# Kernel optimization log

Hardware: AMD Instinct MI355X
Metric: run time of the kernel (lower is better)

## Reference

```python
import math
import jax, jax.numpy as jnp
import numpy as np

B, N, NC = 2, 2048, 256
C_S, C_COND, C_Z, C_H, H, PQK, PV = 384, 256, 128, 16, 12, 4, 8
BQ, BK = 32, 128
NBLK = N // BQ
INF, EPS = 1e5, 1e-8
CONCAT = C_Z // 4 + C_H + PV * 4  # per-head output feature dim


def _ln(x, w=None, b=None, eps=1e-5):
    mu = jnp.mean(x, -1, keepdims=True)
    var = jnp.mean((x - mu) ** 2, -1, keepdims=True)
    y = (x - mu) * jax.lax.rsqrt(var + eps)
    if w is not None:
        y = y * w
    if b is not None:
        y = y + b
    return y


def _quat_to_rot(q):
    w, x, y, z = q[..., 0], q[..., 1], q[..., 2], q[..., 3]
    r = jnp.stack([
        1 - 2 * (y * y + z * z), 2 * (x * y - w * z), 2 * (x * z + w * y),
        2 * (x * y + w * z), 1 - 2 * (x * x + z * z), 2 * (y * z - w * x),
        2 * (x * z - w * y), 2 * (y * z + w * x), 1 - 2 * (x * x + y * y),
    ], axis=-1)
    return r.reshape(q.shape[:-1] + (3, 3))


def setup_inputs() -> dict:
    key = jax.random.key(0)
    ks = jax.random.split(key, 24)
    p = lambda k, shp: 0.02 * jax.random.normal(k, shp, dtype=jnp.float32)
    quat = jax.random.normal(ks[5], (B, N, 4), dtype=jnp.float32)
    quat = quat / jnp.linalg.norm(quat, axis=-1, keepdims=True)
    hc = H * C_H
    return {
        "s": jax.random.normal(ks[0], (B, N, C_S), dtype=jnp.float32),
        "cond": jax.random.normal(ks[1], (B, NC, C_COND), dtype=jnp.float32),
        "z": jax.random.normal(ks[2], (B, NBLK, BQ, BK, C_Z), dtype=jnp.float32),
        "trans": jax.random.normal(ks[3], (B, N, 3), dtype=jnp.float32),
        "rots": _quat_to_rot(quat),
        "s_mask": jnp.ones((B, N), dtype=jnp.float32),
        "cond_to_s_idx": jax.random.randint(ks[4], (B, N), 0, NC),
        "ln_cond_w": jnp.ones((C_COND,), dtype=jnp.float32),
        "lin_cond_W": p(ks[6], (C_S, C_COND)),
        "lin_cond_b": jnp.zeros((C_S,), dtype=jnp.float32),
        "lin_cond_nb_W": p(ks[7], (C_S, C_COND)),
        "ln_z_w": jnp.ones((C_Z,), dtype=jnp.float32),
        "ln_z_b": jnp.zeros((C_Z,), dtype=jnp.float32),
        "Wq": p(ks[8], (hc, C_S)),
        "Wk": p(ks[9], (hc, C_S)),
        "Wv": p(ks[10], (hc, C_S)),
        "Wqp": p(ks[11], (H * PQK * 3, C_S)),
        "Wkvp": p(ks[12], (H * (PQK + PV) * 3, C_S)),
        "Wb": p(ks[13], (H, C_Z)),
        "Wdz": p(ks[14], (C_Z // 4, C_Z)),
        "head_weights": jnp.full((H,), 0.541324854612918, dtype=jnp.float32),
        "Wout": p(ks[15], (C_S, H * CONCAT)),
    }


def _forward(s, cond, z, trans, rots, s_mask, cond_to_s_idx,
             ln_cond_w, lin_cond_W, lin_cond_b, lin_cond_nb_W, ln_z_w, ln_z_b,
             Wq, Wk, Wv, Wqp, Wkvp, Wb, Wdz, head_weights, Wout):
    # ---- GatherAdaLN ----
    s_n = _ln(s)
    c_n = _ln(cond, ln_cond_w)
    idx3 = jnp.broadcast_to(cond_to_s_idx[..., None], (B, N, C_S))
    gate = jnp.take_along_axis(c_n @ lin_cond_W.T + lin_cond_b, idx3, axis=1) * s_mask[..., None]
    bias = jnp.take_along_axis(c_n @ lin_cond_nb_W.T, idx3, axis=1) * s_mask[..., None]
    s2 = s_n * jax.nn.sigmoid(gate) + bias
    # ---- pair LN ----
    zn = _ln(z, ln_z_w, ln_z_b)
    # ---- block gather (to_queries / to_keys) ----
    pad = (BK - BQ) // 2
    base = jnp.arange(NBLK)[:, None] * BQ + jnp.arange(BK)[None, :] - pad  # [NBLK, BK]
    validk = (base >= 0) & (base < N)
    kidx = jnp.clip(base, 0, N - 1)

    def to_q(x):
        return x.reshape((B, NBLK, BQ) + x.shape[2:])

    def to_k(x):
        g = x[:, kidx]  # [B, NBLK, BK, ...]
        vm = validk.reshape((1, NBLK, BK) + (1,) * (g.ndim - 3)).astype(g.dtype)
        return g * vm

    q_in, k_in = to_q(s2), to_k(s2)
    q_t, q_R = to_q(trans), to_q(rots)
    k_t = to_k(trans)
    k_R = jnp.where(validk[None, :, :, None, None], rots[:, kidx], jnp.eye(3, dtype=rots.dtype))
    # ---- scalar q/k/v ----
    q = (q_in @ Wq.T).reshape(B, NBLK, BQ, H, C_H)
    k = (k_in @ Wk.T).reshape(B, NBLK, BK, H, C_H)
    v = (k_in @ Wv.T).reshape(B, NBLK, BK, H, C_H)
    # ---- point q/k/v in global frames ----
    qp = (q_in @ Wqp.T).reshape(B, NBLK, BQ, H * PQK, 3)
    q_pts = (jnp.einsum('bnqij,bnqpj->bnqpi', q_R, qp) + q_t[..., None, :]).reshape(B, NBLK, BQ, H, PQK, 3)
    kvp = (k_in @ Wkvp.T).reshape(B, NBLK, BK, H * (PQK + PV), 3)
    kv_pts = (jnp.einsum('bnkij,bnkpj->bnkpi', k_R, kvp) + k_t[..., None, :]).reshape(B, NBLK, BK, H, PQK + PV, 3)
    k_pts, v_pts = kv_pts[..., :PQK, :], kv_pts[..., PQK:, :]
    # ---- logits ----
    b_bias = zn @ Wb.T  # [B,NBLK,BQ,BK,H]
    a = jnp.einsum('bnqhc,bnkhc->bnqkh', q, k) * math.sqrt(1.0 / (3 * C_H)) + b_bias * math.sqrt(1.0 / 3)
    # point bias (cdist form)
    pt = -2.0 * jnp.einsum('bnqhpd,bnkhpd->bnqkh', q_pts, k_pts)
    pt = pt + jnp.sum(q_pts ** 2, axis=(-1, -2))[..., None, :]
    pt = pt + jnp.sum(k_pts ** 2, axis=(-1, -2))[..., None, :, :]
    hw = jax.nn.softplus(head_weights) * math.sqrt(1.0 / (3 * (PQK * 9.0 / 2)))
    pt = pt * hw * (-0.5)
    qm = to_q(s_mask[..., None])  # [B,NBLK,BQ,1]
    km = to_k(s_mask[..., None])  # [B,NBLK,BK,1]
    amask = INF * (qm * jnp.swapaxes(km, -1, -2) - 1.0)  # [B,NBLK,BQ,BK]
    a = a + pt + amask[..., None]
    a = jax.nn.softmax(jnp.swapaxes(a, -1, -2), axis=-1)  # [B,NBLK,BQ,H,BK]
    # ---- outputs ----
    o = jnp.einsum('bnqhk,bnkhc->bnqhc', a, v).reshape(B, NBLK, BQ, H * C_H)
    o_pt = jnp.einsum('bnqhk,bnkhvc->bnqhvc', a, v_pts)
    o_pt = jnp.einsum('bnqij,bnqhvi->bnqhvj', q_R, o_pt - q_t[..., None, None, :])  # R^T (p - t)
    o_pt_norm = jnp.sqrt(jnp.sum(o_pt ** 2, -1) + EPS).reshape(B, NBLK, BQ, H * PV)
    o_pt_flat = o_pt.reshape(B, NBLK, BQ, H * PV * 3)
    pair_z = zn @ Wdz.T  # [B,NBLK,BQ,BK,C_Z//4]
    o_pair = jnp.einsum('bnqhk,bnqkc->bnqhc', a, pair_z).reshape(B, NBLK, BQ, H * (C_Z // 4))
    feats = jnp.concatenate([o, o_pt_flat, o_pt_norm, o_pair], axis=-1)
    return (feats @ Wout.T).reshape(B, N, C_S)


def reference(s, cond, z, trans, rots, s_mask, cond_to_s_idx,
              ln_cond_w, lin_cond_W, lin_cond_b, lin_cond_nb_W, ln_z_w, ln_z_b,
              Wq, Wk, Wv, Wqp, Wkvp, Wb, Wdz, head_weights, Wout):
    return _forward(s, cond, z, trans, rots, s_mask, cond_to_s_idx,
                    ln_cond_w, lin_cond_W, lin_cond_b, lin_cond_nb_W, ln_z_w, ln_z_b,
                    Wq, Wk, Wv, Wqp, Wkvp, Wb, Wdz, head_weights, Wout)
```

## Files before the change

### kernel.cpp

```cpp
#include <hip/hip_runtime.h>
#include <math.h>

constexpr int Bv = 2, Nv = 2048, NCv = 256;
constexpr int CSv = 384, CCONDv = 256;
constexpr int CHv = 16, Hv = 12, PQKv = 4, PVv = 8;
constexpr int BQv = 32, BKv = 128, NBLKv = 64;
constexpr int HC = Hv * CHv;
constexpr int QPD = Hv * PQKv * 3;
constexpr int FEAT = 960;
constexpr int PROJW = 1152;
constexpr float S1 = 0.14433756729740643f;
constexpr float S2 = 0.5773502691896258f;
constexpr float HWS = 0.13608276348795434f;

typedef __attribute__((ext_vector_type(8))) short bf16x8;
typedef __attribute__((ext_vector_type(4))) float f32x4;

__device__ __forceinline__ short f2bf(float f) {
    unsigned u = __float_as_uint(f);
    u += 0x7FFF + ((u >> 16) & 1);
    return (short)(u >> 16);
}
__device__ __forceinline__ float bf2f(short s) {
    return __uint_as_float(((unsigned)(unsigned short)s) << 16);
}
__device__ __forceinline__ unsigned pk2(short lo, short hi) {
    return ((unsigned)(unsigned short)lo) | (((unsigned)(unsigned short)hi) << 16);
}

__device__ __forceinline__ float blockReduceSum(float v, volatile float* red, int t, int nthr) {
    #pragma unroll
    for (int off = 32; off > 0; off >>= 1) v += __shfl_down(v, off, 64);
    int wid = t >> 6, lane = t & 63, nw = nthr >> 6;
    __syncthreads();
    if (lane == 0) red[wid] = v;
    __syncthreads();
    float r = 0.f;
    for (int w = 0; w < nw; ++w) r += red[w];
    return r;
}

__global__ __launch_bounds__(256) void k_wcvt(const float* __restrict__ Wq,
                                              const float* __restrict__ Wk,
                                              const float* __restrict__ Wv,
                                              const float* __restrict__ Wqp,
                                              const float* __restrict__ Wkvp,
                                              const float* __restrict__ Wg,
                                              const float* __restrict__ Wnb,
                                              short* __restrict__ wsW,
                                              short* __restrict__ wsW2) {
    int i4 = blockIdx.x * 256 + threadIdx.x;
    int off = i4 * 4;
    const float* src;
    short* dst;
    int rel;
    if (off < 442368) {
        dst = wsW; rel = off;
        if (rel < 73728) src = Wq;
        else if (rel < 147456) { src = Wk; rel -= 73728; }
        else if (rel < 221184) { src = Wv; rel -= 147456; }
        else if (rel < 276480) { src = Wqp; rel -= 221184; }
        else { src = Wkvp; rel -= 276480; }
        float4 v = *(const float4*)(src + rel);
        *(uint2*)(dst + off) = make_uint2(pk2(f2bf(v.x), f2bf(v.y)), pk2(f2bf(v.z), f2bf(v.w)));
    } else if (off < 442368 + 196608) {
        int o2 = off - 442368;
        rel = o2;
        if (rel < 98304) src = Wg; else { src = Wnb; rel -= 98304; }
        float4 v = *(const float4*)(src + rel);
        *(uint2*)(wsW2 + o2) = make_uint2(pk2(f2bf(v.x), f2bf(v.y)), pk2(f2bf(v.z), f2bf(v.w)));
    }
}

__global__ __launch_bounds__(256) void k_gemm_bt(const short* __restrict__ A,
                                                 const short* __restrict__ B,
                                                 float* __restrict__ C,
                                                 int K, int ldc) {
    __shared__ short As[128 * 40];
    __shared__ short Bs[128 * 40];
    int t = threadIdx.x;
    int m0 = blockIdx.x * 128, n0 = blockIdx.y * 128;
    int wv = t >> 6, lane = t & 63, lr = lane & 15, quad = lane >> 4;
    int mq = (wv & 1) * 64, nq = (wv >> 1) * 64;
    f32x4 acc[4][4];
    #pragma unroll
    for (int i = 0; i < 4; ++i)
        #pragma unroll
        for (int j = 0; j < 4; ++j) acc[i][j] = 0;

    int r0 = t >> 2, c8 = (t & 3) * 8;
    int r1 = (t + 256) >> 2, c81 = ((t + 256) & 3) * 8;

    for (int k0 = 0; k0 < K; k0 += 32) {
        uint4 a0 = *(const uint4*)(A + (size_t)(m0 + r0) * K + k0 + c8);
        uint4 a1 = *(const uint4*)(A + (size_t)(m0 + r1) * K + k0 + c81);
        uint4 b0 = *(const uint4*)(B + (size_t)(n0 + r0) * K + k0 + c8);
        uint4 b1 = *(const uint4*)(B + (size_t)(n0 + r1) * K + k0 + c81);
        *(uint4*)&As[r0 * 40 + c8] = a0;
        *(uint4*)&As[r1 * 40 + c81] = a1;
        *(uint4*)&Bs[r0 * 40 + c8] = b0;
        *(uint4*)&Bs[r1 * 40 + c81] = b1;
        __syncthreads();
        bf16x8 af[4], bf[4];
        #pragma unroll
        for (int i = 0; i < 4; ++i) {
            af[i] = *(const bf16x8*)&As[(mq + i * 16 + lr) * 40 + quad * 8];
            bf[i] = *(const bf16x8*)&Bs[(nq + i * 16 + lr) * 40 + quad * 8];
        }
        #pragma unroll
        for (int i = 0; i < 4; ++i)
            #pragma unroll
            for (int j = 0; j < 4; ++j)
                acc[i][j] = __builtin_amdgcn_mfma_f32_16x16x32_bf16(af[i], bf[j], acc[i][j], 0, 0, 0);
        __syncthreads();
    }
    #pragma unroll
    for (int i = 0; i < 4; ++i) {
        #pragma unroll
        for (int j = 0; j < 4; ++j) {
            int col = n0 + nq + j * 16 + lr;
            #pragma unroll
            for (int r = 0; r < 4; ++r) {
                int row = m0 + mq + i * 16 + quad * 4 + r;
                C[(size_t)row * ldc + col] = acc[i][j][r];
            }
        }
    }
}

__global__ __launch_bounds__(256) void k_condln(const float* __restrict__ cond,
                                                const float* __restrict__ lnw,
                                                short* __restrict__ cnbf) {
    __shared__ float red[4];
    int row = blockIdx.x;
    int t = threadIdx.x;
    float c = cond[row * CCONDv + t];
    float mu = blockReduceSum(c, red, t, 256) * (1.f / CCONDv);
    float d = c - mu;
    float var = blockReduceSum(d * d, red, t, 256) * (1.f / CCONDv);
    cnbf[row * CCONDv + t] = f2bf(d * rsqrtf(var + 1e-5f) * lnw[t]);
}

__global__ __launch_bounds__(128) void k_s2(const float* __restrict__ s,
                                            const float* __restrict__ gb,
                                            const float* __restrict__ bg,
                                            const int* __restrict__ cidx,
                                            const float* __restrict__ smask,
                                            short* __restrict__ s2bf) {
    __shared__ float red[4];
    int row = blockIdx.x;
    int t = threadIdx.x;
    const float* sr = s + (size_t)row * CSv;
    float x0 = sr[t], x1 = sr[t + 128], x2 = sr[t + 256];
    float mu = blockReduceSum(x0 + x1 + x2, red, t, 128) * (1.f / CSv);
    float d0 = x0 - mu, d1 = x1 - mu, d2 = x2 - mu;
    float var = blockReduceSum(d0 * d0 + d1 * d1 + d2 * d2, red, t, 128) * (1.f / CSv);
    float rs = rsqrtf(var + 1e-5f);
    int b = row / Nv;
    int ci = cidx[row];
    float m = smask[row];
    const float* gbr = gb + (size_t)(b * NCv + ci) * 768;
    float dd[3] = {d0, d1, d2};
    #pragma unroll
    for (int j = 0; j < 3; ++j) {
        int cc = t + j * 128;
        float sn = dd[j] * rs;
        float g = (gbr[cc] + bg[cc]) * m, bi = gbr[384 + cc] * m;
        s2bf[(size_t)row * CSv + cc] = f2bf(sn * (1.f / (1.f + expf(-g))) + bi);
    }
}

__global__ __launch_bounds__(192) void k_post(const float* __restrict__ proj,
                                              const float* __restrict__ rots,
                                              const float* __restrict__ trans,
                                              float* __restrict__ qpts,
                                              float* __restrict__ kpts,
                                              float* __restrict__ vpts,
                                              float* __restrict__ qsq,
                                              float* __restrict__ ksq) {
    __shared__ float R[9], tr[3];
    int row = blockIdx.x;
    int t = threadIdx.x;
    if (t < 9) R[t] = rots[(size_t)row * 9 + t];
    if (t < 3) tr[t] = trans[(size_t)row * 3 + t];
    __syncthreads();
    const float* pr = proj + (size_t)row * PROJW + 576;
    float x = pr[t * 3 + 0], y = pr[t * 3 + 1], z = pr[t * 3 + 2];
    float ox = R[0] * x + R[1] * y + R[2] * z + tr[0];
    float oy = R[3] * x + R[4] * y + R[5] * z + tr[1];
    float oz = R[6] * x + R[7] * y + R[8] * z + tr[2];
    float sq = ox * ox + oy * oy + oz * oz;
    if (t < 48) {
        qpts[(size_t)row * QPD + t * 3 + 0] = ox;
        qpts[(size_t)row * QPD + t * 3 + 1] = oy;
        qpts[(size_t)row * QPD + t * 3 + 2] = oz;
        float s4 = sq + __shfl_xor(sq, 1, 64);
        s4 += __shfl_xor(s4, 2, 64);
        if ((t & 3) == 0) qsq[(size_t)row * Hv + (t >> 2)] = s4;
    } else {
        int p = t - 48;
        int h = p / 12, pp = p % 12;
        if (pp < PQKv) {
            kpts[(size_t)row * QPD + (h * PQKv + pp) * 3 + 0] = ox;
            kpts[(size_t)row * QPD + (h * PQKv + pp) * 3 + 1] = oy;
            kpts[(size_t)row * QPD + (h * PQKv + pp) * 3 + 2] = oz;
            float s4 = sq + __shfl_xor(sq, 1, 64);
            s4 += __shfl_xor(s4, 2, 64);
            if (pp == 0) ksq[(size_t)row * Hv + h] = s4;
        } else {
            int vi = h * PVv + pp - PQKv;
            vpts[(size_t)row * (Hv * PVv * 3) + vi * 3 + 0] = ox;
            vpts[(size_t)row * (Hv * PVv * 3) + vi * 3 + 1] = oy;
            vpts[(size_t)row * (Hv * PVv * 3) + vi * 3 + 2] = oz;
        }
    }
}

__global__ __launch_bounds__(256) void k_prep(const float* __restrict__ Wb,
                                              const float* __restrict__ Wdz,
                                              const float* __restrict__ lnw,
                                              const float* __restrict__ lnb,
                                              short* __restrict__ wp,
                                              float* __restrict__ SB) {
    int t = threadIdx.x;
    if (t < 176) {
        int c = t >> 2, q = t & 3;
        const float* wrow = (c < 12) ? (Wb + (size_t)c * 128) : (Wdz + (size_t)(c - 12) * 128);
        float sacc = 0.f, bacc = 0.f;
        for (int i = q * 32; i < q * 32 + 32; ++i) {
            float wf = wrow[i] * lnw[i];
            short bs = f2bf(wf);
            wp[c * 128 + i] = bs;
            sacc += bf2f(bs);
            bacc += lnb[i] * wrow[i];
        }
        sacc += __shfl_xor(sacc, 1, 64); sacc += __shfl_xor(sacc, 2, 64);
        bacc += __shfl_xor(bacc, 1, 64); bacc += __shfl_xor(bacc, 2, 64);
        if (q == 0) { SB[c] = sacc; SB[48 + c] = bacc; }
    }
    for (int i = t; i < 512; i += 256) wp[44 * 128 + i] = 0;
    if (t >= 176 && t < 180) { SB[t - 132] = 0.f; SB[48 + t - 132] = 0.f; }
}

__global__ __launch_bounds__(256) void k_zproj2(const float* __restrict__ z,
                                                const short* __restrict__ wp,
                                                const float* __restrict__ SB,
                                                short* __restrict__ bbias2,
                                                short* __restrict__ pairzT) {
    __shared__ short zbuf[128 * 136];
    __shared__ short wbuf[48 * 136];
    __shared__ float muL[128], rsL[128], SL[48], BL[48];
    int t = threadIdx.x;
    int bid = blockIdx.x;
    int bblk = bid >> 5, qq = bid & 31;
    size_t row0 = (size_t)bid * 128;

    for (int idx = t; idx < 768; idx += 256) {
        int c = idx >> 4, k8 = idx & 15;
        uint4 v = *(const uint4*)(wp + c * 128 + k8 * 8);
        *(uint4*)&wbuf[c * 136 + k8 * 8] = v;
    }
    if (t < 96) {
        float v = SB[t];
        if (t < 48) SL[t] = v; else BL[t - 48] = v;
    }

    const float4* zsrc = (const float4*)(z + row0 * 128);
    #pragma unroll
    for (int it = 0; it < 16; ++it) {
        int f = it * 256 + t;
        int r = f >> 5, c4 = f & 31;
        float4 v = zsrc[f];
        short s0 = f2bf(v.x), s1 = f2bf(v.y), s2v = f2bf(v.z), s3 = f2bf(v.w);
        *(uint2*)&zbuf[r * 136 + c4 * 4] = make_uint2(pk2(s0, s1), pk2(s2v, s3));
        float sm = v.x + v.y + v.z + v.w;
        float sq = v.x * v.x + v.y * v.y + v.z * v.z + v.w * v.w;
        #pragma unroll
        for (int off = 1; off <= 16; off <<= 1) {
            sm += __shfl_xor(sm, off, 64);
            sq += __shfl_xor(sq, off, 64);
        }
        if ((t & 31) == 0) {
            float mu = sm * (1.f / 128.f);
            float var = sq * (1.f / 128.f) - mu * mu;
            muL[r] = mu;
            rsL[r] = rsqrtf(var + 1e-5f);
        }
    }
    __syncthreads();

    int wv = t >> 6, lane = t & 63;
    int lr = lane & 15, quad = lane >> 4;
    int mb = wv * 32;
    f32x4 acc[2][3];
    #pragma unroll
    for (int i = 0; i < 2; ++i)
        #pragma unroll
        for (int j = 0; j < 3; ++j) acc[i][j] = 0;
    #pragma unroll
    for (int kt = 0; kt < 4; ++kt) {
        int ko = kt * 32 + quad * 8;
        bf16x8 a0 = *(const bf16x8*)&zbuf[(mb + lr) * 136 + ko];
        bf16x8 a1 = *(const bf16x8*)&zbuf[(mb + 16 + lr) * 136 + ko];
        bf16x8 b0 = *(const bf16x8*)&wbuf[lr * 136 + ko];
        bf16x8 b1 = *(const bf16x8*)&wbuf[(16 + lr) * 136 + ko];
        bf16x8 b2 = *(const bf16x8*)&wbuf[(32 + lr) * 136 + ko];
        acc[0][0] = __builtin_amdgcn_mfma_f32_16x16x32_bf16(a0, b0, acc[0][0], 0, 0, 0);
        acc[0][1] = __builtin_amdgcn_mfma_f32_16x16x32_bf16(a0, b1, acc[0][1], 0, 0, 0);
        acc[0][2] = __builtin_amdgcn_mfma_f32_16x16x32_bf16(a0, b2, acc[0][2], 0, 0, 0);
        acc[1][0] = __builtin_amdgcn_mfma_f32_16x16x32_bf16(a1, b0, acc[1][0], 0, 0, 0);
        acc[1][1] = __builtin_amdgcn_mfma_f32_16x16x32_bf16(a1, b1, acc[1][1], 0, 0, 0);
        acc[1][2] = __builtin_amdgcn_mfma_f32_16x16x32_bf16(a1, b2, acc[1][2], 0, 0, 0);
    }

    short* bb_base = bbias2 + (size_t)(bblk * 12) * 4096 + qq * 128;
    short* pz_base = pairzT + (size_t)bid * 32 * 128;
    #pragma unroll
    for (int mt = 0; mt < 2; ++mt) {
        #pragma unroll
        for (int nt = 0; nt < 3; ++nt) {
            int col = nt * 16 + lr;
            int kbase = mb + mt * 16 + quad * 4;
            float ov[4];
            #pragma unroll
            for (int r4 = 0; r4 < 4; ++r4) {
                int rl = kbase + r4;
                ov[r4] = rsL[rl] * (acc[mt][nt][r4] - muL[rl] * SL[col]) + BL[col];
            }
            if (col < 12) {
                *(uint2*)&bb_base[(size_t)col * 4096 + kbase] =
                    make_uint2(pk2(f2bf(S2 * ov[0]), f2bf(S2 * ov[1])),
                               pk2(f2bf(S2 * ov[2]), f2bf(S2 * ov[3])));
            } else if (col < 44) {
                int c = col - 12;
                *(uint2*)&pz_base[c * 128 + kbase] =
                    make_uint2(pk2(f2bf(ov[0]), f2bf(ov[1])), pk2(f2bf(ov[2]), f2bf(ov[3])));
            }
        }
    }
}

__global__ __launch_bounds__(512, 6) void k_attn_main(const float* __restrict__ proj,
                                                      const float* __restrict__ qpts,
                                                      const float* __restrict__ kpts,
                                                      const float* __restrict__ vpts,
                                                      const float* __restrict__ qsq,
                                                      const float* __restrict__ ksq,
                                                      const short* __restrict__ bbias2,
                                                      const float* __restrict__ smask,
                                                      const float* __restrict__ head_w,
                                                      short* __restrict__ Aws,
                                                      float* __restrict__ optraw,
                                                      float* __restrict__ feats) {
    __shared__ short kfrag[128 * 40];
    __shared__ short qfrag[32 * 40];
    __shared__ short vtileT[48 * 136];
    __shared__ float sc[32 * 132];
    __shared__ short Abuf[32 * 136];
    __shared__ float rowb[32], qmL[32], colb[128], kmL[128];
    __shared__ int   nkgL[128];

    int t = threadIdx.x;
    int hp = blockIdx.x % 6;
    int bblk = blockIdx.x / 6;
    int b = bblk >> 6, blk = bblk & 63;
    int wv = t >> 6, lane = t & 63;
    int lr = lane & 15, quad = lane >> 4;

    if (t < 128) {
        int nkrel = blk * BQv + t - 48;
        bool valid = (nkrel >= 0) && (nkrel < Nv);
        int nkg = valid ? (b * Nv + nkrel) : -1;
        nkgL[t] = nkg;
        kmL[t] = valid ? smask[nkg] : 0.f;
    }
    {
        int c = 40 + (t >> 6), k2 = (t & 63) * 2;
        *(unsigned*)&vtileT[c * 136 + k2] = 0;
    }
    __syncthreads();

    for (int hh = 0; hh < 2; ++hh) {
        int h = hp * 2 + hh;
        float hw = log1pf(expf(head_w[h])) * HWS;

        {
            int k = t >> 2, c4 = (t & 3) << 2;
            int g = nkgL[k];
            float4 v = (g >= 0) ? *(const float4*)&proj[(size_t)g * PROJW + 192 + h * 16 + c4]
                                : make_float4(0, 0, 0, 0);
            *(uint2*)&kfrag[k * 40 + c4] =
                make_uint2(pk2(f2bf(v.x), f2bf(v.y)), pk2(f2bf(v.z), f2bf(v.w)));
            kfrag[k * 40 + 28 + (t & 3)] = 0;
        }
        if (t < 384) {
            int k = t / 3, c4 = (t % 3) * 4;
            int g = nkgL[k];
            float4 v = (g >= 0) ? *(const float4*)&kpts[(size_t)g * QPD + h * 12 + c4]
                                : make_float4(0, 0, 0, 0);
            *(uint2*)&kfrag[k * 40 + 16 + c4] =
                make_uint2(pk2(f2bf(v.x), f2bf(v.y)), pk2(f2bf(v.z), f2bf(v.w)));
        }
        if (t < 128) {
            int g = nkgL[t];
            colb[t] = (g >= 0) ? (-0.5f * hw * ksq[(size_t)g * Hv + h]) : 0.f;
            int q = t >> 2, c4 = (t & 3) << 2;
            int nqg = b * Nv + blk * BQv + q;
            float4 v = *(const float4*)&proj[(size_t)nqg * PROJW + h * 16 + c4];
            *(uint2*)&qfrag[q * 40 + c4] =
                make_uint2(pk2(f2bf(S1 * v.x), f2bf(S1 * v.y)),
                           pk2(f2bf(S1 * v.z), f2bf(S1 * v.w)));
            qfrag[q * 40 + 28 + (t & 3)] = 0;
        }
        if (t < 96) {
            int q = t / 3, c4 = (t % 3) * 4;
            int nqg = b * Nv + blk * BQv + q;
            float4 v = *(const float4*)&qpts[(size_t)nqg * QPD + h * 12 + c4];
            *(uint2*)&qfrag[q * 40 + 16 + c4] =
                make_uint2(pk2(f2bf(hw * v.x), f2bf(hw * v.y)),
                           pk2(f2bf(hw * v.z), f2bf(hw * v.w)));
        }
        if (t < 32) {
            int nqg = b * Nv + blk * BQv + t;
            rowb[t] = -0.5f * hw * qsq[(size_t)nqg * Hv + t >= 0 ? (size_t)nqg * Hv + h - ((size_t)nqg * Hv + h) + (size_t)nqg * Hv + h : 0];
            rowb[t] = -0.5f * hw * qsq[(size_t)nqg * Hv + h];
            qmL[t] = smask[nqg];
        }
        {
            int k = t >> 2, c0 = (t & 3) << 2;
            int g = nkgL[k];
            float4 v = (g >= 0) ? *(const float4*)&proj[(size_t)g * PROJW + 384 + h * 16 + c0]
                                : make_float4(0, 0, 0, 0);
            vtileT[(c0 + 0) * 136 + k] = f2bf(v.x);
            vtileT[(c0 + 1) * 136 + k] = f2bf(v.y);
            vtileT[(c0 + 2) * 136 + k] = f2bf(v.z);
            vtileT[(c0 + 3) * 136 + k] = f2bf(v.w);
        }
        for (int i = t; i < 768; i += 512) {
            int k = i / 6, p = i % 6;
            int g = nkgL[k];
            float4 v = (g >= 0) ? *(const float4*)&vpts[(size_t)g * (Hv * PVv * 3) + h * 24 + p * 4]
                                : make_float4(0, 0, 0, 0);
            int c0 = 16 + p * 4;
            vtileT[(c0 + 0) * 136 + k] = f2bf(v.x);
            vtileT[(c0 + 1) * 136 + k] = f2bf(v.y);
            vtileT[(c0 + 2) * 136 + k] = f2bf(v.z);
            vtileT[(c0 + 3) * 136 + k] = f2bf(v.w);
        }
        __syncthreads();

        f32x4 d[2];
        d[0] = 0; d[1] = 0;
        {
            bf16x8 bfr = *(const bf16x8*)&kfrag[(wv * 16 + lr) * 40 + quad * 8];
            bf16x8 a0 = *(const bf16x8*)&qfrag[lr * 40 + quad * 8];
            bf16x8 a1 = *(const bf16x8*)&qfrag[(16 + lr) * 40 + quad * 8];
            d[0] = __builtin_amdgcn_mfma_f32_16x16x32_bf16(a0, bfr, d[0], 0, 0, 0);
            d[1] = __builtin_amdgcn_mfma_f32_16x16x32_bf16(a1, bfr, d[1], 0, 0, 0);
        }
        {
            const short* bb = bbias2 + (size_t)(bblk * 12 + h) * 4096;
            #pragma unroll
            for (int mt = 0; mt < 2; ++mt) {
                #pragma unroll
                for (int r = 0; r < 4; ++r) {
                    int q = mt * 16 + quad * 4 + r;
                    int k = wv * 16 + lr;
                    float logit = d[mt][r] + rowb[q] + colb[k]
                                + 1e5f * (qmL[q] * kmL[k] - 1.f)
                                + bf2f(bb[q * 128 + k]);
                    sc[q * 132 + k] = logit;
                }
            }
        }
        __syncthreads();

        {
            int q = t >> 4, i0 = (t & 15) * 8;
            float v[8];
            float m = -3.0e38f;
            #pragma unroll
            for (int j = 0; j < 8; ++j) { v[j] = sc[q * 132 + i0 + j]; m = fmaxf(m, v[j]); }
            #pragma unroll
            for (int off = 1; off <= 8; off <<= 1) m = fmaxf(m, __shfl_xor(m, off, 64));
            float ssum = 0.f;
            #pragma unroll
            for (int j = 0; j < 8; ++j) { v[j] = __expf(v[j] - m); ssum += v[j]; }
            #pragma unroll
            for (int off = 1; off <= 8; off <<= 1) ssum += __shfl_xor(ssum, off, 64);
            float inv = 1.f / ssum;
            short a8[8];
            #pragma unroll
            for (int j = 0; j < 8; ++j) a8[j] = f2bf(v[j] * inv);
            uint4 packed = make_uint4(pk2(a8[0], a8[1]), pk2(a8[2], a8[3]),
                                      pk2(a8[4], a8[5]), pk2(a8[6], a8[7]));
            *(uint4*)&Abuf[q * 136 + i0] = packed;
            *(uint4*)&Aws[((size_t)(bblk * 32 + q) * 12 + h) * 128 + i0] = packed;
        }
        __syncthreads();

        if (wv < 6) {
            int mt = wv & 1, nt = wv >> 1;
            f32x4 acc = 0;
            #pragma unroll
            for (int kt = 0; kt < 4; ++kt) {
                bf16x8 a = *(const bf16x8*)&Abuf[(mt * 16 + lr) * 136 + quad * 8 + kt * 32];
                bf16x8 bv = *(const bf16x8*)&vtileT[(nt * 16 + lr) * 136 + quad * 8 + kt * 32];
                acc = __builtin_amdgcn_mfma_f32_16x16x32_bf16(a, bv, acc, 0, 0, 0);
            }
            int c = nt * 16 + lr;
            #pragma unroll
            for (int r = 0; r < 4; ++r) {
                int q = mt * 16 + quad * 4 + r;
                size_t nqg = (size_t)b * Nv + blk * BQv + q;
                if (c < 16) feats[nqg * FEAT + h * 16 + c] = acc[r];
                else if (c < 40) optraw[nqg * 288 + h * 24 + (c - 16)] = acc[r];
            }
        }
        __syncthreads();
    }
}

__global__ __launch_bounds__(64) void k_pair(const short* __restrict__ Aws,
                                             const short* __restrict__ pairzT,
                                             const float* __restrict__ optraw,
                                             const float* __restrict__ rots,
                                             const float* __restrict__ trans,
                                             float* __restrict__ feats) {
    __shared__ float Rt[12];
    int t = threadIdx.x;
    int bid = blockIdx.x;
    int lr = t & 15, quad = t >> 4;

    if (t < 9) Rt[t] = rots[(size_t)bid * 9 + t];
    if (t < 3) Rt[9 + t] = trans[(size_t)bid * 3 + t];
    __syncthreads();

    const short* Ab = Aws + (size_t)bid * 1536;
    const short* Pb = pairzT + (size_t)bid * 4096;
    f32x4 acc0 = 0, acc1 = 0;
    #pragma unroll
    for (int kt = 0; kt < 4; ++kt) {
        int ko = kt * 32 + quad * 8;
        bf16x8 a = 0;
        if (lr < 12) a = *(const bf16x8*)&Ab[lr * 128 + ko];
        bf16x8 b0 = *(const bf16x8*)&Pb[lr * 128 + ko];
        bf16x8 b1 = *(const bf16x8*)&Pb[(16 + lr) * 128 + ko];
        acc0 = __builtin_amdgcn_mfma_f32_16x16x32_bf16(a, b0, acc0, 0, 0, 0);
        acc1 = __builtin_amdgcn_mfma_f32_16x16x32_bf16(a, b1, acc1, 0, 0, 0);
    }
    float* frow = feats + (size_t)bid * FEAT;
    #pragma unroll
    for (int r = 0; r < 4; ++r) {
        int hh = quad * 4 + r;
        if (hh < 12) {
            frow[576 + hh * 32 + lr] = acc0[r];
            frow[576 + hh * 32 + 16 + lr] = acc1[r];
        }
    }

    for (int p = t; p < 96; p += 64) {
        float x = optraw[(size_t)bid * 288 + p * 3 + 0] - Rt[9];
        float y = optraw[(size_t)bid * 288 + p * 3 + 1] - Rt[10];
        float z = optraw[(size_t)bid * 288 + p * 3 + 2] - Rt[11];
        float lx = Rt[0] * x + Rt[3] * y + Rt[6] * z;
        float ly = Rt[1] * x + Rt[4] * y + Rt[7] * z;
        float lz = Rt[2] * x + Rt[5] * y + Rt[8] * z;
        frow[192 + p * 3 + 0] = lx;
        frow[192 + p * 3 + 1] = ly;
        frow[192 + p * 3 + 2] = lz;
        frow[480 + p] = sqrtf(lx * lx + ly * ly + lz * lz + 1e-8f);
    }
}

__global__ __launch_bounds__(256) void k_out(const float* __restrict__ A,
                                             const float* __restrict__ Wo,
                                             float* __restrict__ C) {
    __shared__ float As[32][65];
    __shared__ float Bs[32][65];
    int t = threadIdx.x;
    int m0 = blockIdx.x * 64;
    int c0 = blockIdx.y * 64;
    int tx = t & 15, ty = t >> 4;
    int lr = t >> 2, lk = (t & 3) * 8;
    float acc[4][4] = {};
    for (int k0 = 0; k0 < FEAT; k0 += 32) {
        const float4* ap = (const float4*)(A + (size_t)(m0 + lr) * FEAT + k0 + lk);
        const float4* bp = (const float4*)(Wo + (size_t)(c0 + lr) * FEAT + k0 + lk);
        float4 a0 = ap[0], a1 = ap[1];
        float4 b0 = bp[0], b1 = bp[1];
        As[lk + 0][lr] = a0.x; As[lk + 1][lr] = a0.y; As[lk + 2][lr] = a0.z; As[lk + 3][lr] = a0.w;
        As[lk + 4][lr] = a1.x; As[lk + 5][lr] = a1.y; As[lk + 6][lr] = a1.z; As[lk + 7][lr] = a1.w;
        Bs[lk + 0][lr] = b0.x; Bs[lk + 1][lr] = b0.y; Bs[lk + 2][lr] = b0.z; Bs[lk + 3][lr] = b0.w;
        Bs[lk + 4][lr] = b1.x; Bs[lk + 5][lr] = b1.y; Bs[lk + 6][lr] = b1.z; Bs[lk + 7][lr] = b1.w;
        __syncthreads();
        #pragma unroll
        for (int kk = 0; kk < 32; ++kk) {
            float a4[4], b4[4];
            #pragma unroll
            for (int i = 0; i < 4; ++i) a4[i] = As[kk][ty * 4 + i];
            #pragma unroll
            for (int j = 0; j < 4; ++j) b4[j] = Bs[kk][tx * 4 + j];
            #pragma unroll
            for (int i = 0; i < 4; ++i)
                #pragma unroll
                for (int j = 0; j < 4; ++j) acc[i][j] += a4[i] * b4[j];
        }
        __syncthreads();
    }
    #pragma unroll
    for (int i = 0; i < 4; ++i)
        #pragma unroll
        for (int j = 0; j < 4; ++j)
            C[(size_t)(m0 + ty * 4 + i) * CSv + c0 + tx * 4 + j] = acc[i][j];
}

extern "C" void kernel_launch(void* const* d_in, const int* in_sizes, int n_in,
                              void* d_out, int out_size, void* d_ws, size_t ws_size,
                              hipStream_t stream) {
    const float* s          = (const float*)d_in[0];
    const float* cond       = (const float*)d_in[1];
    const float* z          = (const float*)d_in[2];
    const float* trans      = (const float*)d_in[3];
    const float* rots       = (const float*)d_in[4];
    const float* smask      = (const float*)d_in[5];
    const int*   cidx       = (const int*)d_in[6];
    const float* ln_cond_w  = (const float*)d_in[7];
    const float* lin_cond_W = (const float*)d_in[8];
    const float* lin_cond_b = (const float*)d_in[9];
    const float* lin_cond_nb_W = (const float*)d_in[10];
    const float* ln_z_w     = (const float*)d_in[11];
    const float* ln_z_b     = (const float*)d_in[12];
    const float* Wq         = (const float*)d_in[13];
    const float* Wk         = (const float*)d_in[14];
    const float* Wv         = (const float*)d_in[15];
    const float* Wqp        = (const float*)d_in[16];
    const float* Wkvp       = (const float*)d_in[17];
    const float* Wb         = (const float*)d_in[18];
    const float* Wdz        = (const float*)d_in[19];
    const float* head_w     = (const float*)d_in[20];
    const float* Wout       = (const float*)d_in[21];
    float* out = (float*)d_out;

    float* p = (float*)d_ws;
    short* wp = (short*)p; p += 3072;
    float* SBp = p; p += 96;
    short* wsW  = (short*)p; p += 221184;
    short* wsW2 = (short*)p; p += 98304;
    short* cnbf = (short*)p; p += 65536;
    float* gb   = p; p += (size_t)512 * 768;
    short* s2bf = (short*)p; p += (size_t)Bv * Nv * CSv / 2;
    float* proj = p; p += (size_t)Bv * Nv * PROJW;
    float* qpts = p; p += (size_t)Bv * Nv * QPD;
    float* kpts = p; p += (size_t)Bv * Nv * QPD;
    float* vpts = p; p += (size_t)Bv * Nv * (Hv * PVv * 3);
    float* qsq  = p; p += (size_t)Bv * Nv * Hv;
    float* ksq  = p; p += (size_t)Bv * Nv * Hv;
    short* bbias2 = (short*)p; p += (size_t)128 * 12 * 4096 / 2;
    short* pairzT = (short*)p; p += (size_t)128 * 32 * 32 * 64;
    short* Aws    = (short*)p; p += (size_t)4096 * 12 * 64;
    float* optraw = p; p += (size_t)4096 * 288;
    float* feats  = p; p += (size_t)Bv * Nv * FEAT;

    k_wcvt<<<624, 256, 0, stream>>>(Wq, Wk, Wv, Wqp, Wkvp, lin_cond_W, lin_cond_nb_W,
                                    wsW, wsW2);
    k_prep<<<1, 256, 0, stream>>>(Wb, Wdz, ln_z_w, ln_z_b, wp, SBp);
    k_condln<<<Bv * NCv, 256, 0, stream>>>(cond, ln_cond_w, cnbf);
    k_gemm_bt<<<dim3(4, 6), 256, 0, stream>>>(cnbf, wsW2, gb, CCONDv, 768);
    k_s2<<<Bv * Nv, 128, 0, stream>>>(s, gb, lin_cond_b, cidx, smask, s2bf);
    k_gemm_bt<<<dim3(32, 9), 256, 0, stream>>>(s2bf, wsW, proj, CSv, PROJW);
    k_post<<<Bv * Nv, 192, 0, stream>>>(proj, rots, trans, qpts, kpts, vpts, qsq, ksq);
    k_zproj2<<<Bv * NBLKv * BQv, 256, 0, stream>>>(z, wp, SBp, bbias2, pairzT);
    k_attn_main<<<Bv * NBLKv * 6, 512, 0, stream>>>(proj, qpts, kpts, vpts, qsq, ksq,
                                                    bbias2, smask, head_w, Aws, optraw, feats);
    k_pair<<<Bv * NBLKv * BQv, 64, 0, stream>>>(Aws, pairzT, optraw, rots, trans, feats);
    k_out<<<dim3(64, 6), 256, 0, stream>>>(feats, Wout, out);
}
```

Measured before the change: 616.8 us.

## Fuse setup kernels, merge cond GEMM into z-projection, precompute bf16 K/Q/V tiles

Folds the weight conversion, z-LN weight prep and cond LayerNorm into one launch, and runs the small cond GEMM as extra blocks of the z-projection kernel. Adds a k_kvcache pass that converts K/Q/V and point features to bf16 once per (batch, head) into padded, pre-transposed buffers. The attention kernel then loads those tiles with plain 16-byte copies, avoiding repeated fp32 gathers and conversions across overlapping key windows. It also pads the k_out shared tiles and vectorises their reads. The cost is one extra kernel, extra workspace traffic for the cached buffers, and fewer launches overall.

```diff
diff --git a/kernel.cpp b/kernel.cpp
--- a/kernel.cpp
+++ b/kernel.cpp
@@ -9,6 +9,7 @@
 constexpr int QPD = Hv * PQKv * 3;
 constexpr int FEAT = 960;
 constexpr int PROJW = 1152;
+constexpr int NPAD = 2144;
 constexpr float S1 = 0.14433756729740643f;
 constexpr float S2 = 0.5773502691896258f;
 constexpr float HWS = 0.13608276348795434f;
@@ -27,6 +28,8 @@
 __device__ __forceinline__ unsigned pk2(short lo, short hi) {
     return ((unsigned)(unsigned short)lo) | (((unsigned)(unsigned short)hi) << 16);
 }
+
+union BF8 { short s[8]; bf16x8 v; uint4 u; };
 
 __device__ __forceinline__ float blockReduceSum(float v, volatile float* red, int t, int nthr) {
     #pragma unroll
@@ -40,7 +43,7 @@
     return r;
 }
 
-__global__ __launch_bounds__(256) void k_wcvt(const float* __restrict__ Wq,
+__global__ __launch_bounds__(256) void k_head(const float* __restrict__ Wq,
                                               const float* __restrict__ Wk,
                                               const float* __restrict__ Wv,
                                               const float* __restrict__ Wqp,
@@ -48,27 +51,64 @@
                                               const float* __restrict__ Wg,
                                               const float* __restrict__ Wnb,
                                               short* __restrict__ wsW,
-                                              short* __restrict__ wsW2) {
-    int i4 = blockIdx.x * 256 + threadIdx.x;
-    int off = i4 * 4;
-    const float* src;
-    short* dst;
-    int rel;
-    if (off < 442368) {
-        dst = wsW; rel = off;
-        if (rel < 73728) src = Wq;
-        else if (rel < 147456) { src = Wk; rel -= 73728; }
-        else if (rel < 221184) { src = Wv; rel -= 147456; }
-        else if (rel < 276480) { src = Wqp; rel -= 221184; }
-        else { src = Wkvp; rel -= 276480; }
-        float4 v = *(const float4*)(src + rel);
-        *(uint2*)(dst + off) = make_uint2(pk2(f2bf(v.x), f2bf(v.y)), pk2(f2bf(v.z), f2bf(v.w)));
-    } else if (off < 442368 + 196608) {
-        int o2 = off - 442368;
-        rel = o2;
-        if (rel < 98304) src = Wg; else { src = Wnb; rel -= 98304; }
-        float4 v = *(const float4*)(src + rel);
-        *(uint2*)(wsW2 + o2) = make_uint2(pk2(f2bf(v.x), f2bf(v.y)), pk2(f2bf(v.z), f2bf(v.w)));
+                                              short* __restrict__ wsW2,
+                                              const float* __restrict__ Wb,
+                                              const float* __restrict__ Wdz,
+                                              const float* __restrict__ lnzw,
+                                              const float* __restrict__ lnzb,
+                                              short* __restrict__ wp,
+                                              float* __restrict__ SB,
+                                              const float* __restrict__ cond,
+                                              const float* __restrict__ lncw,
+                                              short* __restrict__ cnbf) {
+    __shared__ float red[4];
+    int bid = blockIdx.x;
+    int t = threadIdx.x;
+    if (bid < 624) {
+        int off = (bid * 256 + t) * 4;
+        const float* src;
+        int rel;
+        if (off < 442368) {
+            rel = off;
+            if (rel < 73728) src = Wq;
+            else if (rel < 147456) { src = Wk; rel -= 73728; }
+            else if (rel < 221184) { src = Wv; rel -= 147456; }
+            else if (rel < 276480) { src = Wqp; rel -= 221184; }
+            else { src = Wkvp; rel -= 276480; }
+            float4 v = *(const float4*)(src + rel);
+            *(uint2*)(wsW + off) = make_uint2(pk2(f2bf(v.x), f2bf(v.y)), pk2(f2bf(v.z), f2bf(v.w)));
+        } else {
+            int o2 = off - 442368;
+            rel = o2;
+            if (rel < 98304) src = Wg; else { src = Wnb; rel -= 98304; }
+            float4 v = *(const float4*)(src + rel);
+            *(uint2*)(wsW2 + o2) = make_uint2(pk2(f2bf(v.x), f2bf(v.y)), pk2(f2bf(v.z), f2bf(v.w)));
+        }
+    } else if (bid == 624) {
+        if (t < 176) {
+            int c = t >> 2, q = t & 3;
+            const float* wrow = (c < 12) ? (Wb + (size_t)c * 128) : (Wdz + (size_t)(c - 12) * 128);
+            float sacc = 0.f, bacc = 0.f;
+            for (int i = q * 32; i < q * 32 + 32; ++i) {
+                float wf = wrow[i] * lnzw[i];
+                short bs = f2bf(wf);
+                wp[c * 128 + i] = bs;
+                sacc += bf2f(bs);
+                bacc += lnzb[i] * wrow[i];
+            }
+            sacc += __shfl_xor(sacc, 1, 64); sacc += __shfl_xor(sacc, 2, 64);
+            bacc += __shfl_xor(bacc, 1, 64); bacc += __shfl_xor(bacc, 2, 64);
+            if (q == 0) { SB[c] = sacc; SB[48 + c] = bacc; }
+        }
+        for (int i = t; i < 512; i += 256) wp[44 * 128 + i] = 0;
+        if (t >= 176 && t < 180) { SB[t - 132] = 0.f; SB[48 + t - 132] = 0.f; }
+    } else {
+        int row = bid - 625;
+        float c = cond[row * CCONDv + t];
+        float mu = blockReduceSum(c, red, t, 256) * (1.f / CCONDv);
+        float d = c - mu;
+        float var = blockReduceSum(d * d, red, t, 256) * (1.f / CCONDv);
+        cnbf[row * CCONDv + t] = f2bf(d * rsqrtf(var + 1e-5f) * lncw[t]);
     }
 }
 
@@ -126,19 +166,6 @@
             }
         }
     }
-}
-
-__global__ __launch_bounds__(256) void k_condln(const float* __restrict__ cond,
-                                                const float* __restrict__ lnw,
-                                                short* __restrict__ cnbf) {
-    __shared__ float red[4];
-    int row = blockIdx.x;
-    int t = threadIdx.x;
-    float c = cond[row * CCONDv + t];
-    float mu = blockReduceSum(c, red, t, 256) * (1.f / CCONDv);
-    float d = c - mu;
-    float var = blockReduceSum(d * d, red, t, 256) * (1.f / CCONDv);
-    cnbf[row * CCONDv + t] = f2bf(d * rsqrtf(var + 1e-5f) * lnw[t]);
 }
 
 __global__ __launch_bounds__(128) void k_s2(const float* __restrict__ s,
@@ -216,42 +243,75 @@
     }
 }
 
-__global__ __launch_bounds__(256) void k_prep(const float* __restrict__ Wb,
-                                              const float* __restrict__ Wdz,
-                                              const float* __restrict__ lnw,
-                                              const float* __restrict__ lnb,
-                                              short* __restrict__ wp,
-                                              float* __restrict__ SB) {
-    int t = threadIdx.x;
-    if (t < 176) {
-        int c = t >> 2, q = t & 3;
-        const float* wrow = (c < 12) ? (Wb + (size_t)c * 128) : (Wdz + (size_t)(c - 12) * 128);
-        float sacc = 0.f, bacc = 0.f;
-        for (int i = q * 32; i < q * 32 + 32; ++i) {
-            float wf = wrow[i] * lnw[i];
-            short bs = f2bf(wf);
-            wp[c * 128 + i] = bs;
-            sacc += bf2f(bs);
-            bacc += lnb[i] * wrow[i];
-        }
-        sacc += __shfl_xor(sacc, 1, 64); sacc += __shfl_xor(sacc, 2, 64);
-        bacc += __shfl_xor(bacc, 1, 64); bacc += __shfl_xor(bacc, 2, 64);
-        if (q == 0) { SB[c] = sacc; SB[48 + c] = bacc; }
-    }
-    for (int i = t; i < 512; i += 256) wp[44 * 128 + i] = 0;
-    if (t >= 176 && t < 180) { SB[t - 132] = 0.f; SB[48 + t - 132] = 0.f; }
-}
-
-__global__ __launch_bounds__(256) void k_zproj2(const float* __restrict__ z,
-                                                const short* __restrict__ wp,
-                                                const float* __restrict__ SB,
-                                                short* __restrict__ bbias2,
-                                                short* __restrict__ pairzT) {
-    __shared__ short zbuf[128 * 136];
-    __shared__ short wbuf[48 * 136];
-    __shared__ float muL[128], rsL[128], SL[48], BL[48];
+__global__ __launch_bounds__(256) void k_zg(const float* __restrict__ z,
+                                            const short* __restrict__ wp,
+                                            const float* __restrict__ SB,
+                                            short* __restrict__ bbias2,
+                                            short* __restrict__ pairzT,
+                                            const short* __restrict__ cnbf,
+                                            const short* __restrict__ wsW2,
+                                            float* __restrict__ gb) {
+    extern __shared__ char smem[];
     int t = threadIdx.x;
     int bid = blockIdx.x;
+    if (bid >= 4096) {
+        short* As = (short*)smem;
+        short* Bs = As + 128 * 40;
+        int g = bid - 4096;
+        int m0 = (g & 3) * 128, n0 = (g >> 2) * 128;
+        const int K = CCONDv, ldc = 768;
+        int wv = t >> 6, lane = t & 63, lr = lane & 15, quad = lane >> 4;
+        int mq = (wv & 1) * 64, nq = (wv >> 1) * 64;
+        f32x4 acc[4][4];
+        #pragma unroll
+        for (int i = 0; i < 4; ++i)
+            #pragma unroll
+            for (int j = 0; j < 4; ++j) acc[i][j] = 0;
+        int r0 = t >> 2, c8 = (t & 3) * 8;
+        int r1 = (t + 256) >> 2, c81 = ((t + 256) & 3) * 8;
+        for (int k0 = 0; k0 < K; k0 += 32) {
+            uint4 a0 = *(const uint4*)(cnbf + (size_t)(m0 + r0) * K + k0 + c8);
+            uint4 a1 = *(const uint4*)(cnbf + (size_t)(m0 + r1) * K + k0 + c81);
+            uint4 b0 = *(const uint4*)(wsW2 + (size_t)(n0 + r0) * K + k0 + c8);
+            uint4 b1 = *(const uint4*)(wsW2 + (size_t)(n0 + r1) * K + k0 + c81);
+            *(uint4*)&As[r0 * 40 + c8] = a0;
+            *(uint4*)&As[r1 * 40 + c81] = a1;
+            *(uint4*)&Bs[r0 * 40 + c8] = b0;
+            *(uint4*)&Bs[r1 * 40 + c81] = b1;
+            __syncthreads();
+            bf16x8 af[4], bf[4];
+            #pragma unroll
+            for (int i = 0; i < 4; ++i) {
+                af[i] = *(const bf16x8*)&As[(mq + i * 16 + lr) * 40 + quad * 8];
+                bf[i] = *(const bf16x8*)&Bs[(nq + i * 16 + lr) * 40 + quad * 8];
+            }
+            #pragma unroll
+            for (int i = 0; i < 4; ++i)
+                #pragma unroll
+                for (int j = 0; j < 4; ++j)
+                    acc[i][j] = __builtin_amdgcn_mfma_f32_16x16x32_bf16(af[i], bf[j], acc[i][j], 0, 0, 0);
+            __syncthreads();
+        }
+        #pragma unroll
+        for (int i = 0; i < 4; ++i)
+            #pragma unroll
+            for (int j = 0; j < 4; ++j) {
+                int col = n0 + nq + j * 16 + lr;
+                #pragma unroll
+                for (int r = 0; r < 4; ++r) {
+                    int row = m0 + mq + i * 16 + quad * 4 + r;
+                    gb[(size_t)row * ldc + col] = acc[i][j][r];
+                }
+            }
+        return;
+    }
+    short* zbuf = (short*)smem;
+    short* wbuf = zbuf + 128 * 136;
+    float* muL  = (float*)(wbuf + 48 * 136);
+    float* rsL  = muL + 128;
+    float* SL   = rsL + 128;
+    float* BL   = SL + 48;
+
     int bblk = bid >> 5, qq = bid & 31;
     size_t row0 = (size_t)bid * 128;
 
@@ -340,15 +400,111 @@
     }
 }
 
-__global__ __launch_bounds__(512, 6) void k_attn_main(const float* __restrict__ proj,
-                                                      const float* __restrict__ qpts,
-                                                      const float* __restrict__ kpts,
-                                                      const float* __restrict__ vpts,
-                                                      const float* __restrict__ qsq,
-                                                      const float* __restrict__ ksq,
+__global__ __launch_bounds__(256) void k_kvcache(const float* __restrict__ proj,
+                                                 const float* __restrict__ qpts,
+                                                 const float* __restrict__ kpts,
+                                                 const float* __restrict__ vpts,
+                                                 const float* __restrict__ qsq,
+                                                 const float* __restrict__ ksq,
+                                                 const float* __restrict__ smask,
+                                                 const float* __restrict__ head_w,
+                                                 short* __restrict__ kc,
+                                                 short* __restrict__ qc,
+                                                 short* __restrict__ vTc,
+                                                 float* __restrict__ cb,
+                                                 float* __restrict__ rb,
+                                                 float* __restrict__ kmp) {
+    __shared__ short vt[40 * 136];
+    int t = threadIdx.x;
+    int tile = blockIdx.x % 17;
+    int bh = blockIdx.x / 17;
+    int b = bh / 12, h = bh % 12;
+    float hw = log1pf(expf(head_w[h])) * HWS;
+    int pn0 = tile * 128;
+    int npn = (pn0 + 128 <= NPAD) ? 128 : (NPAD - pn0);
+
+    for (int i = t; i < npn * 4; i += 256) {
+        int r = i >> 2, q = i & 3;
+        int pn = pn0 + r;
+        int n = pn - 48; n = n < 0 ? 0 : (n > Nv - 1 ? Nv - 1 : n);
+        size_t g = (size_t)b * Nv + n;
+        BF8 o;
+        if (q < 2) {
+            const float* src = proj + g * PROJW + 192 + h * 16 + q * 8;
+            #pragma unroll
+            for (int j = 0; j < 8; ++j) o.s[j] = f2bf(src[j]);
+        } else if (q == 2) {
+            const float* src = kpts + g * QPD + h * 12;
+            #pragma unroll
+            for (int j = 0; j < 8; ++j) o.s[j] = f2bf(src[j]);
+        } else {
+            const float* src = kpts + g * QPD + h * 12 + 8;
+            #pragma unroll
+            for (int j = 0; j < 4; ++j) o.s[j] = f2bf(src[j]);
+            o.s[4] = o.s[5] = o.s[6] = o.s[7] = 0;
+        }
+        *(uint4*)&kc[(((size_t)bh) * NPAD + pn) * 32 + q * 8] = o.u;
+    }
+    for (int i = t; i < npn; i += 256) {
+        int pn = pn0 + i;
+        int n = pn - 48; n = n < 0 ? 0 : (n > Nv - 1 ? Nv - 1 : n);
+        size_t g = (size_t)b * Nv + n;
+        cb[(size_t)bh * NPAD + pn] = -0.5f * hw * ksq[g * Hv + h];
+        if (h == 0) kmp[(size_t)b * NPAD + pn] = (pn >= 48 && pn < 48 + Nv) ? smask[g] : 0.f;
+    }
+    for (int i = t; i < 512; i += 256) {
+        int r = i >> 2, q = i & 3;
+        int n = pn0 - 48 + r;
+        if (n >= 0 && n < Nv) {
+            size_t g = (size_t)b * Nv + n;
+            BF8 o;
+            if (q < 2) {
+                const float* src = proj + g * PROJW + h * 16 + q * 8;
+                #pragma unroll
+                for (int j = 0; j < 8; ++j) o.s[j] = f2bf(S1 * src[j]);
+            } else if (q == 2) {
+                const float* src = qpts + g * QPD + h * 12;
+                #pragma unroll
+                for (int j = 0; j < 8; ++j) o.s[j] = f2bf(hw * src[j]);
+            } else {
+                const float* src = qpts + g * QPD + h * 12 + 8;
+                #pragma unroll
+                for (int j = 0; j < 4; ++j) o.s[j] = f2bf(hw * src[j]);
+                o.s[4] = o.s[5] = o.s[6] = o.s[7] = 0;
+            }
+            *(uint4*)&qc[(((size_t)bh) * Nv + n) * 32 + q * 8] = o.u;
+            if (q == 0) rb[(size_t)bh * Nv + n] = -0.5f * hw * qsq[g * Hv + h];
+        }
+    }
+    for (int i = t; i < npn * 10; i += 256) {
+        int r = i / 10, q = i % 10;
+        int pn = pn0 + r;
+        int n = pn - 48; n = n < 0 ? 0 : (n > Nv - 1 ? Nv - 1 : n);
+        size_t g = (size_t)b * Nv + n;
+        float4 v = (q < 4) ? *(const float4*)&proj[g * PROJW + 384 + h * 16 + q * 4]
+                           : *(const float4*)&vpts[g * (Hv * PVv * 3) + h * 24 + (q - 4) * 4];
+        int c0 = q * 4;
+        vt[(c0 + 0) * 136 + r] = f2bf(v.x);
+        vt[(c0 + 1) * 136 + r] = f2bf(v.y);
+        vt[(c0 + 2) * 136 + r] = f2bf(v.z);
+        vt[(c0 + 3) * 136 + r] = f2bf(v.w);
+    }
+    __syncthreads();
+    for (int i = t; i < 640; i += 256) {
+        int c = i >> 4, s = i & 15;
+        if (s * 8 < npn)
+            *(uint4*)&vTc[((size_t)bh * 40 + c) * NPAD + pn0 + s * 8] = *(const uint4*)&vt[c * 136 + s * 8];
+    }
+}
+
+__global__ __launch_bounds__(512, 6) void k_attn_main(const short* __restrict__ kc,
+                                                      const short* __restrict__ qc,
+                                                      const short* __restrict__ vTc,
+                                                      const float* __restrict__ cb,
+                                                      const float* __restrict__ rb,
+                                                      const float* __restrict__ kmp,
+                                                      const float* __restrict__ smask,
                                                       const short* __restrict__ bbias2,
-                                                      const float* __restrict__ smask,
-                                                      const float* __restrict__ head_w,
                                                       short* __restrict__ Aws,
                                                       float* __restrict__ optraw,
                                                       float* __restrict__ feats) {
@@ -358,7 +514,6 @@
     __shared__ float sc[32 * 132];
     __shared__ short Abuf[32 * 136];
     __shared__ float rowb[32], qmL[32], colb[128], kmL[128];
-    __shared__ int   nkgL[128];
 
     int t = threadIdx.x;
     int hp = blockIdx.x % 6;
@@ -366,14 +521,10 @@
     int b = bblk >> 6, blk = bblk & 63;
     int wv = t >> 6, lane = t & 63;
     int lr = lane & 15, quad = lane >> 4;
-
-    if (t < 128) {
-        int nkrel = blk * BQv + t - 48;
-        bool valid = (nkrel >= 0) && (nkrel < Nv);
-        int nkg = valid ? (b * Nv + nkrel) : -1;
-        nkgL[t] = nkg;
-        kmL[t] = valid ? smask[nkg] : 0.f;
-    }
+    int n0 = blk * BQv;
+
+    if (t < 128) kmL[t] = kmp[(size_t)b * NPAD + n0 + t];
+    if (t < 32)  qmL[t] = smask[(size_t)b * Nv + n0 + t];
     {
         int c = 40 + (t >> 6), k2 = (t & 63) * 2;
         *(unsigned*)&vtileT[c * 136 + k2] = 0;
@@ -382,70 +533,21 @@
 
     for (int hh = 0; hh < 2; ++hh) {
         int h = hp * 2 + hh;
-        float hw = log1pf(expf(head_w[h])) * HWS;
+        size_t bh = (size_t)b * 12 + h;
 
         {
-            int k = t >> 2, c4 = (t & 3) << 2;
-            int g = nkgL[k];
-            float4 v = (g >= 0) ? *(const float4*)&proj[(size_t)g * PROJW + 192 + h * 16 + c4]
-                                : make_float4(0, 0, 0, 0);
-            *(uint2*)&kfrag[k * 40 + c4] =
-                make_uint2(pk2(f2bf(v.x), f2bf(v.y)), pk2(f2bf(v.z), f2bf(v.w)));
-            kfrag[k * 40 + 28 + (t & 3)] = 0;
-        }
-        if (t < 384) {
-            int k = t / 3, c4 = (t % 3) * 4;
-            int g = nkgL[k];
-            float4 v = (g >= 0) ? *(const float4*)&kpts[(size_t)g * QPD + h * 12 + c4]
-                                : make_float4(0, 0, 0, 0);
-            *(uint2*)&kfrag[k * 40 + 16 + c4] =
-                make_uint2(pk2(f2bf(v.x), f2bf(v.y)), pk2(f2bf(v.z), f2bf(v.w)));
+            int r = t >> 2, s8 = (t & 3) * 8;
+            *(uint4*)&kfrag[r * 40 + s8] = *(const uint4*)&kc[(bh * NPAD + n0 + r) * 32 + s8];
         }
         if (t < 128) {
-            int g = nkgL[t];
-            colb[t] = (g >= 0) ? (-0.5f * hw * ksq[(size_t)g * Hv + h]) : 0.f;
-            int q = t >> 2, c4 = (t & 3) << 2;
-            int nqg = b * Nv + blk * BQv + q;
-            float4 v = *(const float4*)&proj[(size_t)nqg * PROJW + h * 16 + c4];
-            *(uint2*)&qfrag[q * 40 + c4] =
-                make_uint2(pk2(f2bf(S1 * v.x), f2bf(S1 * v.y)),
-                           pk2(f2bf(S1 * v.z), f2bf(S1 * v.w)));
-            qfrag[q * 40 + 28 + (t & 3)] = 0;
-        }
-        if (t < 96) {
-            int q = t / 3, c4 = (t % 3) * 4;
-            int nqg = b * Nv + blk * BQv + q;
-            float4 v = *(const float4*)&qpts[(size_t)nqg * QPD + h * 12 + c4];
-            *(uint2*)&qfrag[q * 40 + 16 + c4] =
-                make_uint2(pk2(f2bf(hw * v.x), f2bf(hw * v.y)),
-                           pk2(f2bf(hw * v.z), f2bf(hw * v.w)));
-        }
-        if (t < 32) {
-            int nqg = b * Nv + blk * BQv + t;
-            rowb[t] = -0.5f * hw * qsq[(size_t)nqg * Hv + t >= 0 ? (size_t)nqg * Hv + h - ((size_t)nqg * Hv + h) + (size_t)nqg * Hv + h : 0];
-            rowb[t] = -0.5f * hw * qsq[(size_t)nqg * Hv + h];
-            qmL[t] = smask[nqg];
-        }
-        {
-            int k = t >> 2, c0 = (t & 3) << 2;
-            int g = nkgL[k];
-            float4 v = (g >= 0) ? *(const float4*)&proj[(size_t)g * PROJW + 384 + h * 16 + c0]
-                                : make_float4(0, 0, 0, 0);
-            vtileT[(c0 + 0) * 136 + k] = f2bf(v.x);
-            vtileT[(c0 + 1) * 136 + k] = f2bf(v.y);
-            vtileT[(c0 + 2) * 136 + k] = f2bf(v.z);
-            vtileT[(c0 + 3) * 136 + k] = f2bf(v.w);
-        }
-        for (int i = t; i < 768; i += 512) {
-            int k = i / 6, p = i % 6;
-            int g = nkgL[k];
-            float4 v = (g >= 0) ? *(const float4*)&vpts[(size_t)g * (Hv * PVv * 3) + h * 24 + p * 4]
-                                : make_float4(0, 0, 0, 0);
-            int c0 = 16 + p * 4;
-            vtileT[(c0 + 0) * 136 + k] = f2bf(v.x);
-            vtileT[(c0 + 1) * 136 + k] = f2bf(v.y);
-            vtileT[(c0 + 2) * 136 + k] = f2bf(v.z);
-            vtileT[(c0 + 3) * 136 + k] = f2bf(v.w);
+            int r = t >> 2, s8 = (t & 3) * 8;
+            *(uint4*)&qfrag[r * 40 + s8] = *(const uint4*)&qc[(bh * Nv + n0 + r) * 32 + s8];
+        }
+        if (t < 128) colb[t] = cb[bh * NPAD + n0 + t];
+        if (t < 32)  rowb[t] = rb[bh * Nv + n0 + t];
+        for (int i = t; i < 640; i += 512) {
+            int c = i >> 4, s8 = (i & 15) * 8;
+            *(uint4*)&vtileT[c * 136 + s8] = *(const uint4*)&vTc[(bh * 40 + c) * NPAD + n0 + s8];
         }
         __syncthreads();
 
@@ -512,7 +614,7 @@
             #pragma unroll
             for (int r = 0; r < 4; ++r) {
                 int q = mt * 16 + quad * 4 + r;
-                size_t nqg = (size_t)b * Nv + blk * BQv + q;
+                size_t nqg = (size_t)b * Nv + n0 + q;
                 if (c < 16) feats[nqg * FEAT + h * 16 + c] = acc[r];
                 else if (c < 40) optraw[nqg * 288 + h * 24 + (c - 16)] = acc[r];
             }
@@ -576,8 +678,8 @@
 __global__ __launch_bounds__(256) void k_out(const float* __restrict__ A,
                                              const float* __restrict__ Wo,
                                              float* __restrict__ C) {
-    __shared__ float As[32][65];
-    __shared__ float Bs[32][65];
+    __shared__ float As[32][68];
+    __shared__ float Bs[32][68];
     int t = threadIdx.x;
     int m0 = blockIdx.x * 64;
     int c0 = blockIdx.y * 64;
@@ -596,15 +698,14 @@
         __syncthreads();
         #pragma unroll
         for (int kk = 0; kk < 32; ++kk) {
-            float a4[4], b4[4];
-            #pragma unroll
-            for (int i = 0; i < 4; ++i) a4[i] = As[kk][ty * 4 + i];
-            #pragma unroll
-            for (int j = 0; j < 4; ++j) b4[j] = Bs[kk][tx * 4 + j];
+            float4 a4 = *(const float4*)&As[kk][ty * 4];
+            float4 b4 = *(const float4*)&Bs[kk][tx * 4];
+            float av[4] = {a4.x, a4.y, a4.z, a4.w};
+            float bv[4] = {b4.x, b4.y, b4.z, b4.w};
             #pragma unroll
             for (int i = 0; i < 4; ++i)
                 #pragma unroll
-                for (int j = 0; j < 4; ++j) acc[i][j] += a4[i] * b4[j];
+                for (int j = 0; j < 4; ++j) acc[i][j] += av[i] * bv[j];
         }
         __syncthreads();
     }
@@ -661,18 +762,24 @@
     short* Aws    = (short*)p; p += (size_t)4096 * 12 * 64;
     float* optraw = p; p += (size_t)4096 * 288;
     float* feats  = p; p += (size_t)Bv * Nv * FEAT;
-
-    k_wcvt<<<624, 256, 0, stream>>>(Wq, Wk, Wv, Wqp, Wkvp, lin_cond_W, lin_cond_nb_W,
-                                    wsW, wsW2);
-    k_prep<<<1, 256, 0, stream>>>(Wb, Wdz, ln_z_w, ln_z_b, wp, SBp);
-    k_condln<<<Bv * NCv, 256, 0, stream>>>(cond, ln_cond_w, cnbf);
-    k_gemm_bt<<<dim3(4, 6), 256, 0, stream>>>(cnbf, wsW2, gb, CCONDv, 768);
+    short* kc  = (short*)p; p += (size_t)Bv * 12 * NPAD * 32 / 2;
+    short* qc  = (short*)p; p += (size_t)Bv * 12 * Nv * 32 / 2;
+    short* vTc = (short*)p; p += (size_t)Bv * 12 * 40 * NPAD / 2;
+    float* cbw = p; p += (size_t)Bv * 12 * NPAD;
+    float* rbw = p; p += (size_t)Bv * 12 * Nv;
+    float* kmp = p; p += (size_t)Bv * NPAD;
+
+    k_head<<<1137, 256, 0, stream>>>(Wq, Wk, Wv, Wqp, Wkvp, lin_cond_W, lin_cond_nb_W,
+                                     wsW, wsW2, Wb, Wdz, ln_z_w, ln_z_b, wp, SBp,
+                                     cond, ln_cond_w, cnbf);
+    k_zg<<<4120, 256, 49280, stream>>>(z, wp, SBp, bbias2, pairzT, cnbf, wsW2, gb);
     k_s2<<<Bv * Nv, 128, 0, stream>>>(s, gb, lin_cond_b, cidx, smask, s2bf);
     k_gemm_bt<<<dim3(32, 9), 256, 0, stream>>>(s2bf, wsW, proj, CSv, PROJW);
     k_post<<<Bv * Nv, 192, 0, stream>>>(proj, rots, trans, qpts, kpts, vpts, qsq, ksq);
-    k_zproj2<<<Bv * NBLKv * BQv, 256, 0, stream>>>(z, wp, SBp, bbias2, pairzT);
-    k_attn_main<<<Bv * NBLKv * 6, 512, 0, stream>>>(proj, qpts, kpts, vpts, qsq, ksq,
-                                                    bbias2, smask, head_w, Aws, optraw, feats);
+    k_kvcache<<<Bv * 12 * 17, 256, 0, stream>>>(proj, qpts, kpts, vpts, qsq, ksq,
+                                                smask, head_w, kc, qc, vTc, cbw, rbw, kmp);
+    k_attn_main<<<Bv * NBLKv * 6, 512, 0, stream>>>(kc, qc, vTc, cbw, rbw, kmp, smask,
+                                                    bbias2, Aws, optraw, feats);
     k_pair<<<Bv * NBLKv * BQv, 64, 0, stream>>>(Aws, pairzT, optraw, rots, trans, feats);
     k_out<<<dim3(64, 6), 256, 0, stream>>>(feats, Wout, out);
 }
```

After: 580.3 us. -5.9%, faster.
